# Performance work log

Measured on AMD Instinct MI355X. Metric: run time of the kernel, lower is better.

The kernel has to match this reference:

```python
import jax, jax.numpy as jnp
import numpy as np

EPS = 1e-8

def spatial_similarity(x):
    # x: [B, C, H, W] -> similarity [B, 1, HW, HW]
    b, c = x.shape[0], x.shape[1]
    fm = x.reshape(b, c, -1)                                   # [B, C, HW]
    norm_fm = fm / (jnp.sqrt(jnp.sum(fm * fm, axis=1, keepdims=True)) + EPS)
    s = jnp.einsum('bcn,bcm->bnm', norm_fm, norm_fm)            # [B, HW, HW]
    return s[:, None]                                           # [B, 1, HW, HW]

def l1_loss(a, b):
    return jnp.mean(jnp.abs(a - b))

def setup_inputs() -> dict:
    key = jax.random.key(0)
    k0, k1, k2, k3 = jax.random.split(key, 4)
    shape = (8, 128, 48, 48)
    return {
        'outputs0': jax.random.normal(k0, shape, dtype=jnp.float32),
        'outputs1': jax.random.normal(k1, shape, dtype=jnp.float32),
        'targets0': jax.random.normal(k2, shape, dtype=jnp.float32),
        'targets1': jax.random.normal(k3, shape, dtype=jnp.float32),
    }

def reference(outputs0, outputs1, targets0, targets1):
    # stu_ch == tea_ch -> random index slice is identity (index = 0)
    loss = l1_loss(spatial_similarity(outputs0), spatial_similarity(targets0))
    loss = loss + l1_loss(spatial_similarity(outputs1), spatial_similarity(targets1))
    return loss
```

## Files before the change

### kernel.cpp

```cpp
#include <hip/hip_runtime.h>
#include <hip/hip_bf16.h>
#include <stdint.h>

#define B_DIM 8
#define C_DIM 128
#define N_SP 2304
#define NT 18
#define NTRI 171
#define NTILES (2 * B_DIM * NTRI)
#define GRID_G (NTILES / 2)

typedef __attribute__((ext_vector_type(8))) short short8;
typedef __attribute__((ext_vector_type(4))) float f32x4;

__device__ __forceinline__ uint32_t f2bf(float f) {
    uint32_t u = __float_as_uint(f);
    return (u + 0x7fffu + ((u >> 16) & 1u)) >> 16;
}

__global__ __launch_bounds__(256) void prep_kernel(
    const float* __restrict__ x0, const float* __restrict__ x1,
    const float* __restrict__ x2, const float* __restrict__ x3,
    ushort* __restrict__ xt, float* __restrict__ rinv, float* __restrict__ accum)
{
    __shared__ ushort stage[64 * 128];

    int bid = blockIdx.x;
    if (bid == 0 && threadIdx.x < 64) accum[threadIdx.x] = 0.f;
    int t  = bid / 288;
    int b  = (bid / 36) % 8;
    int nb = bid % 36;
    int tid = threadIdx.x;
    int q   = tid & 3;
    int nl  = tid >> 2;
    int n   = nb * 64 + nl;
    const float* x  = t == 0 ? x0 : t == 1 ? x1 : t == 2 ? x2 : x3;
    const float* xb = x + (size_t)b * (C_DIM * N_SP) + n;
    int sw = nl & 7;

    float s = 0.f;
#pragma unroll
    for (int jj = 0; jj < 4; ++jj) {
        uint32_t w[4];
#pragma unroll
        for (int m = 0; m < 4; ++m) {
            int c = q * 32 + jj * 8 + m * 2;
            float v0 = xb[(size_t)c * N_SP];
            float v1 = xb[(size_t)(c + 1) * N_SP];
            s = fmaf(v0, v0, s);
            s = fmaf(v1, v1, s);
            w[m] = f2bf(v0) | (f2bf(v1) << 16);
        }
        int J = q * 4 + jj;
        uint4 u; u.x = w[0]; u.y = w[1]; u.z = w[2]; u.w = w[3];
        *(uint4*)&stage[nl * 128 + ((J ^ sw) * 8)] = u;
    }
    s += __shfl_xor(s, 1, 64);
    s += __shfl_xor(s, 2, 64);
    if (q == 0) rinv[(size_t)(t * 8 + b) * N_SP + n] = 1.f / (sqrtf(s) + 1e-8f);

    __syncthreads();
    ushort* dst = xt + ((size_t)(t * 8 + b) * N_SP + (size_t)nb * 64) * 128;
#pragma unroll
    for (int it = 0; it < 4; ++it)
        *(uint4*)(dst + it * 2048 + tid * 8) = *(const uint4*)(stage + it * 2048 + tid * 8);
}

struct TileInfo {
    const ushort* xo; const ushort* xg;
    const float*  ro; const float*  rg;
    int tn, tm; float w2; int pair;
};

__device__ __forceinline__ TileInfo decode_tile(int g, const ushort* xt, const float* rinv) {
    int pair = g / (B_DIM * NTRI);
    int rem  = g - pair * (B_DIM * NTRI);
    int b    = rem / NTRI;
    int t    = rem - b * NTRI;
    int tn = 0, cnt = NT;
    while (t >= cnt) { t -= cnt; --cnt; ++tn; }
    TileInfo ti;
    ti.tn = tn; ti.tm = tn + t;
    ti.xo = xt + (size_t)(pair * 8 + b) * N_SP * 128;
    ti.xg = xt + (size_t)((pair + 2) * 8 + b) * N_SP * 128;
    ti.ro = rinv + (size_t)(pair * 8 + b) * N_SP;
    ti.rg = rinv + (size_t)((pair + 2) * 8 + b) * N_SP;
    ti.w2 = (tn == ti.tm) ? 1.f : 2.f;
    ti.pair = pair;
    return ti;
}

#define STAGE(sbase, TN, TM, h, PA, PB)                                             \
    {                                                                               \
        const ushort* sb = (wid & 2) ? (sbase) + (size_t)(TM) * 16384               \
                                     : (sbase) + (size_t)(TN) * 16384;              \
        ushort* pp = (wid & 2) ? (PB) : (PA);                                       \
        int i0 = (wid & 1) * 8;                                                     \
        _Pragma("unroll")                                                           \
        for (int i = 0; i < 8; ++i) {                                               \
            int ii = i0 + i;                                                        \
            int col = ii * 8 + (lane >> 3);                                         \
            const ushort* src = sb + (size_t)col * 128 + (h) * 64 + (lane & 7) * 8; \
            __builtin_amdgcn_global_load_lds(                                       \
                (const __attribute__((address_space(1))) uint32_t*)src,             \
                (__attribute__((address_space(3))) uint32_t*)(pp + ii * 512),       \
                16, 0, 0);                                                          \
        }                                                                           \
    }

#define COMPUTE(ACC, PA, PB)                                                        \
    _Pragma("unroll")                                                               \
    for (int s = 0; s < 2; ++s) {                                                   \
        short8 av[4], bv[4];                                                        \
        int g = lane >> 4;                                                          \
        _Pragma("unroll")                                                           \
        for (int i = 0; i < 4; ++i) {                                               \
            int ca = wrow * 64 + i * 16 + (lane & 15);                              \
            av[i] = *(const short8*)&(PA)[ca * 64 + ((s * 4 + g) ^ (ca & 7)) * 8];  \
            int cb = wcol * 64 + i * 16 + (lane & 15);                              \
            bv[i] = *(const short8*)&(PB)[cb * 64 + ((s * 4 + g) ^ (cb & 7)) * 8];  \
        }                                                                           \
        _Pragma("unroll")                                                           \
        for (int i = 0; i < 4; ++i)                                                 \
            _Pragma("unroll")                                                       \
            for (int j = 0; j < 4; ++j)                                             \
                ACC[i][j] = __builtin_amdgcn_mfma_f32_16x16x32_bf16(                \
                    av[i], bv[j], ACC[i][j], 0, 0, 0);                              \
    }

#define ZERO_ACC()                                                                  \
    _Pragma("unroll")                                                               \
    for (int i = 0; i < 4; ++i)                                                     \
        _Pragma("unroll")                                                           \
        for (int j = 0; j < 4; ++j) {                                               \
            acc_o[i][j] = (f32x4){0.f, 0.f, 0.f, 0.f};                              \
            acc_t[i][j] = (f32x4){0.f, 0.f, 0.f, 0.f};                              \
        }

#define EPILOGUE(Q, W2)                                                             \
    {                                                                               \
        int fr = lane & 15, fq = lane >> 4;                                         \
        float co[4], cg[4];                                                         \
        _Pragma("unroll")                                                           \
        for (int j = 0; j < 4; ++j) {                                               \
            co[j] = rn[Q][1][wcol * 64 + j * 16 + fr];                              \
            cg[j] = rn[Q][3][wcol * 64 + j * 16 + fr];                              \
        }                                                                           \
        float lsum = 0.f;                                                           \
        _Pragma("unroll")                                                           \
        for (int i = 0; i < 4; ++i) {                                               \
            _Pragma("unroll")                                                       \
            for (int r = 0; r < 4; ++r) {                                           \
                int rowl = wrow * 64 + i * 16 + fq * 4 + r;                         \
                float ror = rn[Q][0][rowl], rgr = rn[Q][2][rowl];                   \
                _Pragma("unroll")                                                   \
                for (int j = 0; j < 4; ++j) {                                       \
                    float so = acc_o[i][j][r] * ror * co[j];                        \
                    float st = acc_t[i][j][r] * rgr * cg[j];                        \
                    lsum += fabsf(so - st);                                         \
                }                                                                   \
            }                                                                       \
        }                                                                           \
        lsum *= (W2);                                                               \
        _Pragma("unroll")                                                           \
        for (int off = 32; off > 0; off >>= 1) lsum += __shfl_down(lsum, off, 64);  \
        if (lane == 0) wred[wid] = lsum;                                            \
    }

__global__ __launch_bounds__(256, 2) void gram_kernel(
    const ushort* __restrict__ xt, const float* __restrict__ rinv,
    float* __restrict__ accum)
{
    __shared__ ushort pA[2][128 * 64];
    __shared__ ushort pB[2][128 * 64];
    __shared__ float rn[2][4][128];
    __shared__ float wred[4];

    int bid0 = blockIdx.x;
    int bid  = (bid0 & 7) * (GRID_G / 8) + (bid0 >> 3);

    TileInfo t0 = decode_tile(2 * bid,     xt, rinv);
    TileInfo t1 = decode_tile(2 * bid + 1, xt, rinv);

    int tid  = threadIdx.x;
    int wid  = tid >> 6;
    int lane = tid & 63;
    int wrow = wid >> 1, wcol = wid & 1;

    f32x4 acc_o[4][4], acc_t[4][4];
    ZERO_ACC();

    STAGE(t0.xo, t0.tn, t0.tm, 0, pA[0], pB[0]);
    if (tid < 128) {
        rn[0][0][tid] = t0.ro[t0.tn * 128 + tid];
        rn[0][1][tid] = t0.ro[t0.tm * 128 + tid];
        rn[1][0][tid] = t1.ro[t1.tn * 128 + tid];
        rn[1][1][tid] = t1.ro[t1.tm * 128 + tid];
    } else {
        int u = tid - 128;
        rn[0][2][u] = t0.rg[t0.tn * 128 + u];
        rn[0][3][u] = t0.rg[t0.tm * 128 + u];
        rn[1][2][u] = t1.rg[t1.tn * 128 + u];
        rn[1][3][u] = t1.rg[t1.tm * 128 + u];
    }
    __syncthreads();
    STAGE(t0.xo, t0.tn, t0.tm, 1, pA[1], pB[1]);
    COMPUTE(acc_o, pA[0], pB[0]);
    __syncthreads();
    STAGE(t0.xg, t0.tn, t0.tm, 0, pA[0], pB[0]);
    COMPUTE(acc_o, pA[1], pB[1]);
    __syncthreads();
    STAGE(t0.xg, t0.tn, t0.tm, 1, pA[1], pB[1]);
    COMPUTE(acc_t, pA[0], pB[0]);
    __syncthreads();
    STAGE(t1.xo, t1.tn, t1.tm, 0, pA[0], pB[0]);
    COMPUTE(acc_t, pA[1], pB[1]);
    EPILOGUE(0, t0.w2);
    ZERO_ACC();
    __syncthreads();
    if (tid == 0)
        atomicAdd(&accum[t0.pair * 32 + (bid0 & 31)],
                  wred[0] + wred[1] + wred[2] + wred[3]);
    STAGE(t1.xo, t1.tn, t1.tm, 1, pA[1], pB[1]);
    COMPUTE(acc_o, pA[0], pB[0]);
    __syncthreads();
    STAGE(t1.xg, t1.tn, t1.tm, 0, pA[0], pB[0]);
    COMPUTE(acc_o, pA[1], pB[1]);
    __syncthreads();
    STAGE(t1.xg, t1.tn, t1.tm, 1, pA[1], pB[1]);
    COMPUTE(acc_t, pA[0], pB[0]);
    __syncthreads();
    COMPUTE(acc_t, pA[1], pB[1]);
    EPILOGUE(1, t1.w2);
    __syncthreads();
    if (tid == 0)
        atomicAdd(&accum[t1.pair * 32 + (bid0 & 31)],
                  wred[0] + wred[1] + wred[2] + wred[3]);
}

__global__ void finalize_kernel(const float* __restrict__ a, float* __restrict__ out) {
    float s = a[threadIdx.x];
#pragma unroll
    for (int off = 32; off > 0; off >>= 1) s += __shfl_down(s, off, 64);
    if (threadIdx.x == 0) out[0] = s * (1.0f / 42467328.0f);
}

extern "C" void kernel_launch(void* const* d_in, const int* in_sizes, int n_in,
                              void* d_out, int out_size, void* d_ws, size_t ws_size,
                              hipStream_t stream) {
    const float* o0 = (const float*)d_in[0];
    const float* o1 = (const float*)d_in[1];
    const float* t0 = (const float*)d_in[2];
    const float* t1 = (const float*)d_in[3];

    ushort* xtw  = (ushort*)d_ws;
    float*  rinv = (float*)((char*)d_ws + (size_t)4 * 8 * N_SP * 256);
    float*  accum = rinv + 4 * 8 * N_SP;

    prep_kernel<<<1152, 256, 0, stream>>>(o0, o1, t0, t1, xtw, rinv, accum);
    gram_kernel<<<GRID_G, 256, 0, stream>>>(xtw, rinv, accum);
    finalize_kernel<<<1, 64, 0, stream>>>(accum, (float*)d_out);
}
```

Before: 121.5 us.

## Replace full syncthreads with raw barriers and partial vmcnt waits in gram pipeline

Swaps each __syncthreads between staging and compute for a pair of raw s_barrier calls with a vmcnt(8) wait, so the next stage's global loads can stay in flight while the current buffer is consumed. Each wave now keeps its reduced partial sum in a register and issues its own atomicAdd, which removes the shared-memory cross-wave reduction and its extra barriers. The cost is four times as many atomics. Correctness depends on STAGE issuing exactly the assumed number of vector memory ops (and on how they reach LDS), so the hand-written waitcnt may be fragile.

```diff
diff --git a/kernel.cpp b/kernel.cpp
--- a/kernel.cpp
+++ b/kernel.cpp
@@ -137,7 +137,7 @@
             acc_t[i][j] = (f32x4){0.f, 0.f, 0.f, 0.f};                              \
         }
 
-#define EPILOGUE(Q, W2)                                                             \
+#define EPILOGUE_REG(Q, W2, OUT)                                                    \
     {                                                                               \
         int fr = lane & 15, fq = lane >> 4;                                         \
         float co[4], cg[4];                                                         \
@@ -164,8 +164,12 @@
         lsum *= (W2);                                                               \
         _Pragma("unroll")                                                           \
         for (int off = 32; off > 0; off >>= 1) lsum += __shfl_down(lsum, off, 64);  \
-        if (lane == 0) wred[wid] = lsum;                                            \
-    }
+        OUT = lsum;                                                                 \
+    }
+
+#define RBAR()    __builtin_amdgcn_s_barrier()
+#define WAIT8()   asm volatile("s_waitcnt vmcnt(8)" ::: "memory")
+#define WAIT0()   asm volatile("s_waitcnt vmcnt(0)" ::: "memory")
 
 __global__ __launch_bounds__(256, 2) void gram_kernel(
     const ushort* __restrict__ xt, const float* __restrict__ rinv,
@@ -174,7 +178,6 @@
     __shared__ ushort pA[2][128 * 64];
     __shared__ ushort pB[2][128 * 64];
     __shared__ float rn[2][4][128];
-    __shared__ float wred[4];
 
     int bid0 = blockIdx.x;
     int bid  = (bid0 & 7) * (GRID_G / 8) + (bid0 >> 3);
@@ -189,6 +192,7 @@
 
     f32x4 acc_o[4][4], acc_t[4][4];
     ZERO_ACC();
+    float sum0, sum1;
 
     STAGE(t0.xo, t0.tn, t0.tm, 0, pA[0], pB[0]);
     if (tid < 128) {
@@ -206,36 +210,48 @@
     __syncthreads();
     STAGE(t0.xo, t0.tn, t0.tm, 1, pA[1], pB[1]);
     COMPUTE(acc_o, pA[0], pB[0]);
-    __syncthreads();
+
+    RBAR();
     STAGE(t0.xg, t0.tn, t0.tm, 0, pA[0], pB[0]);
+    WAIT8(); RBAR();
     COMPUTE(acc_o, pA[1], pB[1]);
-    __syncthreads();
+
+    RBAR();
     STAGE(t0.xg, t0.tn, t0.tm, 1, pA[1], pB[1]);
+    WAIT8(); RBAR();
     COMPUTE(acc_t, pA[0], pB[0]);
-    __syncthreads();
+
+    RBAR();
     STAGE(t1.xo, t1.tn, t1.tm, 0, pA[0], pB[0]);
+    WAIT8(); RBAR();
     COMPUTE(acc_t, pA[1], pB[1]);
-    EPILOGUE(0, t0.w2);
+    EPILOGUE_REG(0, t0.w2, sum0);
     ZERO_ACC();
-    __syncthreads();
-    if (tid == 0)
-        atomicAdd(&accum[t0.pair * 32 + (bid0 & 31)],
-                  wred[0] + wred[1] + wred[2] + wred[3]);
+
+    RBAR();
     STAGE(t1.xo, t1.tn, t1.tm, 1, pA[1], pB[1]);
+    WAIT8(); RBAR();
     COMPUTE(acc_o, pA[0], pB[0]);
-    __syncthreads();
+
+    RBAR();
     STAGE(t1.xg, t1.tn, t1.tm, 0, pA[0], pB[0]);
+    WAIT8(); RBAR();
     COMPUTE(acc_o, pA[1], pB[1]);
-    __syncthreads();
+
+    RBAR();
     STAGE(t1.xg, t1.tn, t1.tm, 1, pA[1], pB[1]);
+    WAIT8(); RBAR();
     COMPUTE(acc_t, pA[0], pB[0]);
-    __syncthreads();
+
+    RBAR();
+    WAIT0(); RBAR();
     COMPUTE(acc_t, pA[1], pB[1]);
-    EPILOGUE(1, t1.w2);
-    __syncthreads();
-    if (tid == 0)
-        atomicAdd(&accum[t1.pair * 32 + (bid0 & 31)],
-                  wred[0] + wred[1] + wred[2] + wred[3]);
+    EPILOGUE_REG(1, t1.w2, sum1);
+
+    if (lane == 0) {
+        atomicAdd(&accum[t0.pair * 32 + (bid0 & 31)], sum0);
+        atomicAdd(&accum[t1.pair * 32 + (bid0 & 31)], sum1);
+    }
 }
 
 __global__ void finalize_kernel(const float* __restrict__ a, float* __restrict__ out) {
```

Result: slower. 167.2 us (+37.6%).
